# Optimization experiments

Hardware: AMD Instinct MI355X
Metric: run time of the kernel (lower is better)

The kernel has to match this reference:

```python
import jax, jax.numpy as jnp
import numpy as np

C = 256
NUM_GROUPS = 32
EPS = 1e-5


def group_norm(x, gamma, beta):
    # x: [B, C, H, W]; normalize within each of NUM_GROUPS channel groups
    B, Cc, H, W = x.shape
    xg = x.reshape(B, NUM_GROUPS, Cc // NUM_GROUPS, H, W)
    mean = xg.mean(axis=(2, 3, 4), keepdims=True)
    var = xg.var(axis=(2, 3, 4), keepdims=True)
    xg = (xg - mean) * jax.lax.rsqrt(var + EPS)
    x = xg.reshape(B, Cc, H, W)
    return x * gamma[None, :, None, None] + beta[None, :, None, None]


def conv1x1(x, w, b):
    # w: [C_out, C_in], b: [C_out]; equivalent to nn.Conv2d(k=1)
    return jnp.einsum('oc,bchw->bohw', w, x) + b[None, :, None, None]


def setup_inputs() -> dict:
    key = jax.random.key(0)
    ks = jax.random.split(key, 12)
    B, H, W = 8, 64, 64
    x = jax.random.normal(ks[0], (B, C, H, W), dtype=jnp.float32)
    temb = jax.random.normal(ks[1], (B, 512), dtype=jnp.float32)
    s = 1.0 / np.sqrt(C)  # kaiming-uniform-ish scale for 1x1 conv
    def wmat(k):
        return jax.random.uniform(k, (C, C), dtype=jnp.float32, minval=-s, maxval=s)
    def bvec(k):
        return jax.random.uniform(k, (C,), dtype=jnp.float32, minval=-s, maxval=s)
    return {
        'x': x, 'temb': temb,
        'gn_w': jnp.ones((C,), jnp.float32), 'gn_b': jnp.zeros((C,), jnp.float32),
        'wq': wmat(ks[2]), 'bq': bvec(ks[3]),
        'wk': wmat(ks[4]), 'bk': bvec(ks[5]),
        'wv': wmat(ks[6]), 'bv': bvec(ks[7]),
        'wp': wmat(ks[8]), 'bp': bvec(ks[9]),
    }


def reference(x, temb, gn_w, gn_b, wq, bq, wk, bk, wv, bv, wp, bp):
    B, Cc, H, W = x.shape
    h = group_norm(x, gn_w, gn_b)
    q = conv1x1(h, wq, bq)
    k = conv1x1(h, wk, bk)
    v = conv1x1(h, wv, bv)
    # full self-attention over spatial positions: scores [B, H, W, H, W]
    scale = Cc ** (-0.5)
    w = jnp.einsum('bchw,bcij->bhwij', q, k) * scale
    w = jax.nn.softmax(w.reshape(B, H, W, H * W), axis=-1).reshape(B, H, W, H, W)
    h = jnp.einsum('bhwij,bcij->bchw', w, v)
    h = conv1x1(h, wp, bp)
    return (x + h, temb)
```

## Files before the change

kernel.cpp:

```cpp
#include <hip/hip_runtime.h>
#include <hip/hip_bf16.h>

#define B_ 8
#define C_ 256
#define S_ 4096
#define G_ 32
#define GC_ 8
#define EPS_ 1e-5f

typedef __attribute__((ext_vector_type(4))) float f32x4;
typedef __attribute__((ext_vector_type(8))) short bf16x8;
typedef __attribute__((ext_vector_type(4))) short bf16x4;
typedef __attribute__((ext_vector_type(4))) unsigned int u32x4;
typedef __attribute__((ext_vector_type(2))) unsigned int u32x2;

#define DI __device__ __forceinline__

DI unsigned short f2bf(float f) {
    union { float f; unsigned u; } v; v.f = f;
    unsigned r = v.u + 0x7fffu + ((v.u >> 16) & 1u);
    return (unsigned short)(r >> 16);
}

DI unsigned cvt_pk_bf16(float lo, float hi) {
    unsigned r;
    asm("v_cvt_pk_bf16_f32 %0, %1, %2" : "=v"(r) : "v"(lo), "v"(hi));
    return r;
}

__global__ __launch_bounds__(256) void k_gn_stats(const float* __restrict__ x,
                                                  float* __restrict__ stats) {
    int bg = blockIdx.x;
    const float4* xp = (const float4*)(x + (size_t)bg * (GC_ * S_));
    float s = 0.f, ss = 0.f;
    for (int i = threadIdx.x; i < GC_ * S_ / 4; i += 256) {
        float4 v = xp[i];
        s  += v.x + v.y + v.z + v.w;
        ss += v.x * v.x + v.y * v.y + v.z * v.z + v.w * v.w;
    }
    #pragma unroll
    for (int off = 32; off; off >>= 1) { s += __shfl_down(s, off); ss += __shfl_down(ss, off); }
    __shared__ float rs[4], rss[4];
    int w = threadIdx.x >> 6;
    if ((threadIdx.x & 63) == 0) { rs[w] = s; rss[w] = ss; }
    __syncthreads();
    if (threadIdx.x == 0) {
        float S1 = rs[0] + rs[1] + rs[2] + rs[3];
        float S2 = rss[0] + rss[1] + rss[2] + rss[3];
        float inv = 1.f / (GC_ * S_);
        float mean = S1 * inv;
        float var = S2 * inv - mean * mean;
        stats[bg * 2] = mean;
        stats[bg * 2 + 1] = rsqrtf(var + EPS_);
    }
}

__global__ __launch_bounds__(256) void k_gn_apply(const float* __restrict__ x,
                                                  const float* __restrict__ stats,
                                                  const float* __restrict__ gw,
                                                  const float* __restrict__ gb,
                                                  unsigned short* __restrict__ h) {
    int b = blockIdx.x >> 6;
    int s0 = (blockIdx.x & 63) * 64;
    __shared__ unsigned short tile[64 * 256];
    const float* xb = x + (size_t)b * C_ * S_;
    for (int id = threadIdx.x; id < 256 * 16; id += 256) {
        int c = id >> 4, s4 = id & 15;
        float4 v = *(const float4*)(xb + (size_t)c * S_ + s0 + s4 * 4);
        float mean = stats[(b * G_ + (c >> 3)) * 2];
        float rstd = stats[(b * G_ + (c >> 3)) * 2 + 1];
        float ga = gw[c], be = gb[c];
        float vv[4] = {v.x, v.y, v.z, v.w};
        #pragma unroll
        for (int i = 0; i < 4; i++) {
            int srow = s4 * 4 + i;
            unsigned byte = srow * 512u + c * 2u;
            byte ^= ((srow & 7u) << 4);
            *(unsigned short*)((char*)tile + byte) = f2bf((vv[i] - mean) * rstd * ga + be);
        }
    }
    __syncthreads();
    unsigned short* hb = h + (size_t)b * S_ * C_;
    for (int id = threadIdx.x; id < 2048; id += 256) {
        int srow = id >> 5, ck = id & 31;
        unsigned byte = srow * 512u + ck * 16u;
        byte ^= ((srow & 7u) << 4);
        u32x4 v = *(u32x4*)((char*)tile + byte);
        *(u32x4*)(hb + (size_t)(s0 + srow) * C_ + ck * 8) = v;
    }
}

template <int MODE>
__global__ __launch_bounds__(256) void k_gemm(const float* __restrict__ W,
                                              const float* __restrict__ bias,
                                              const unsigned short* __restrict__ Bm,
                                              unsigned short* __restrict__ outb,
                                              float* __restrict__ outf,
                                              const float* __restrict__ xres,
                                              float qscale) {
    int n0 = (blockIdx.x & 31) * 128;
    int m0 = ((blockIdx.x >> 5) & 1) * 128;
    int b = blockIdx.x >> 6;
    __shared__ unsigned short Alds[128 * 64];
    __shared__ unsigned short Blds[128 * 64];
    int tid = threadIdx.x;
    int lane = tid & 63, wv = tid >> 6;
    int wm = (wv >> 1) * 64, wn = (wv & 1) * 64;
    int lr = lane & 15, lg = lane >> 4;
    f32x4 acc[4][4] = {};
    const unsigned short* Bb = Bm + (size_t)b * S_ * C_;

    for (int k0 = 0; k0 < 256; k0 += 64) {
        __syncthreads();
        {
            int row = tid >> 1, half = tid & 1;
            const float* src = W + (size_t)(m0 + row) * C_ + k0 + half * 32;
            unsigned short tmp[32];
            #pragma unroll
            for (int i = 0; i < 8; i++) {
                float4 v = *(const float4*)(src + i * 4);
                tmp[i * 4 + 0] = f2bf(v.x); tmp[i * 4 + 1] = f2bf(v.y);
                tmp[i * 4 + 2] = f2bf(v.z); tmp[i * 4 + 3] = f2bf(v.w);
            }
            #pragma unroll
            for (int i = 0; i < 4; i++) {
                unsigned byte = row * 128u + half * 64u + i * 16u;
                byte ^= ((row & 7u) << 4);
                *(u32x4*)((char*)Alds + byte) = *(u32x4*)(tmp + i * 8);
            }
        }
        #pragma unroll
        for (int i = 0; i < 4; i++) {
            int id = tid + i * 256;
            int row = id >> 3, ck = id & 7;
            u32x4 v = *(const u32x4*)(Bb + (size_t)(n0 + row) * C_ + k0 + ck * 8);
            unsigned byte = row * 128u + ck * 16u;
            byte ^= ((row & 7u) << 4);
            *(u32x4*)((char*)Blds + byte) = v;
        }
        __syncthreads();
        #pragma unroll
        for (int ks = 0; ks < 2; ks++) {
            bf16x8 af[4], bf[4];
            #pragma unroll
            for (int mf = 0; mf < 4; mf++) {
                int m = wm + mf * 16 + lr;
                unsigned byte = m * 128u + ks * 64u + lg * 16u;
                byte ^= ((m & 7u) << 4);
                af[mf] = *(bf16x8*)((char*)Alds + byte);
            }
            #pragma unroll
            for (int nf = 0; nf < 4; nf++) {
                int n = wn + nf * 16 + lr;
                unsigned byte = n * 128u + ks * 64u + lg * 16u;
                byte ^= ((n & 7u) << 4);
                bf[nf] = *(bf16x8*)((char*)Blds + byte);
            }
            #pragma unroll
            for (int mf = 0; mf < 4; mf++)
                #pragma unroll
                for (int nf = 0; nf < 4; nf++)
                    acc[mf][nf] = __builtin_amdgcn_mfma_f32_16x16x32_bf16(af[mf], bf[nf], acc[mf][nf], 0, 0, 0);
        }
    }

    if (MODE == 0 || MODE == 1) {
        unsigned short* ob = outb + (size_t)b * S_ * C_;
        #pragma unroll
        for (int mf = 0; mf < 4; mf++)
            #pragma unroll
            for (int nf = 0; nf < 4; nf++) {
                int cbase = m0 + wm + mf * 16 + lg * 4;
                int srow = n0 + wn + nf * 16 + lr;
                bf16x4 pk;
                #pragma unroll
                for (int r = 0; r < 4; r++) {
                    float v = acc[mf][nf][r] + bias[cbase + r];
                    if (MODE == 0) v *= qscale;
                    pk[r] = (short)f2bf(v);
                }
                *(bf16x4*)(ob + (size_t)srow * C_ + cbase) = pk;
            }
    } else if (MODE == 2) {
        unsigned short* ob = outb + (size_t)b * C_ * S_;
        #pragma unroll
        for (int mf = 0; mf < 4; mf++)
            #pragma unroll
            for (int nf = 0; nf < 4; nf++)
                #pragma unroll
                for (int r = 0; r < 4; r++) {
                    int c = m0 + wm + mf * 16 + lg * 4 + r;
                    int s = n0 + wn + nf * 16 + lr;
                    ob[(size_t)c * S_ + s] = f2bf(acc[mf][nf][r] + bias[c]);
                }
    } else {
        float* ob = outf + (size_t)b * C_ * S_;
        const float* xb = xres + (size_t)b * C_ * S_;
        #pragma unroll
        for (int mf = 0; mf < 4; mf++)
            #pragma unroll
            for (int nf = 0; nf < 4; nf++)
                #pragma unroll
                for (int r = 0; r < 4; r++) {
                    int c = m0 + wm + mf * 16 + lg * 4 + r;
                    int s = n0 + wn + nf * 16 + lr;
                    ob[(size_t)c * S_ + s] = acc[mf][nf][r] + bias[c] + xb[(size_t)c * S_ + s];
                }
    }
}

__global__ __launch_bounds__(512, 2) void k_attn(const unsigned short* __restrict__ Q,
                                                 const unsigned short* __restrict__ K,
                                                 const unsigned short* __restrict__ V,
                                                 unsigned short* __restrict__ O) {
    int b = blockIdx.x & 7;
    int q0 = (blockIdx.x >> 3) * 128;
    int tid = threadIdx.x, lane = tid & 63, wv = tid >> 6;
    int lr = lane & 15, lg = lane >> 4;
    int qg = wv & 3, kg = wv >> 2;
    int qw = q0 + qg * 32;
    __shared__ unsigned short Klds[64 * 256];
    __shared__ unsigned short Vlds[256 * 64];
    __shared__ unsigned short Plds[4][32 * 64];
    __shared__ float mlp[8 * 2 * 16];
    const unsigned short* Qb = Q + (size_t)b * S_ * C_;
    const unsigned short* Kb = K + (size_t)b * S_ * C_;
    const unsigned short* Vb = V + (size_t)b * C_ * S_;

    bf16x8 qf_[8][2];
    #pragma unroll
    for (int ks = 0; ks < 8; ks++)
        #pragma unroll
        for (int qf = 0; qf < 2; qf++)
            qf_[ks][qf] = *(const bf16x8*)(Qb + (size_t)(qw + qf * 16 + lr) * C_ + ks * 32 + lg * 8);

    unsigned kaddr[2][8];
    #pragma unroll
    for (int kf = 0; kf < 2; kf++) {
        int key = kg * 32 + kf * 16 + lr;
        #pragma unroll
        for (int ks = 0; ks < 8; ks++)
            kaddr[kf][ks] = (unsigned)key * 512u + (((unsigned)(4 * ks + lg + 2 * key) & 31u) << 4);
    }

    f32x4 acc[8][2] = {};
    float lrun[2] = {0.f, 0.f};

    int krow[4], kck[4], vc[4], vck[4];
    #pragma unroll
    for (int i = 0; i < 4; i++) {
        int id = tid + i * 512;
        krow[i] = id >> 5; kck[i] = id & 31;
        vc[i] = id >> 3;  vck[i] = id & 7;
    }
    unsigned kwb[4], vwb[4];
    #pragma unroll
    for (int i = 0; i < 4; i++) {
        kwb[i] = krow[i] * 512u + (((unsigned)(kck[i] + 2 * krow[i]) & 31u) << 4);
        vwb[i] = vc[i] * 128u + ((vck[i] * 16u) ^ ((vc[i] & 7u) << 4));
    }

    u32x4 kpre[4], vpre[4];
    #pragma unroll
    for (int i = 0; i < 4; i++) {
        kpre[i] = *(const u32x4*)(Kb + (size_t)krow[i] * C_ + kck[i] * 8);
        vpre[i] = *(const u32x4*)(Vb + (size_t)vc[i] * S_ + vck[i] * 8);
    }
    #pragma unroll
    for (int i = 0; i < 4; i++) {
        *(u32x4*)((char*)Klds + kwb[i]) = kpre[i];
        *(u32x4*)((char*)Vlds + vwb[i]) = vpre[i];
    }
    __syncthreads();

    for (int kt = 0; kt < 64; kt++) {
        bool pf = (kt + 1) < 64;
        if (pf) {
            #pragma unroll
            for (int i = 0; i < 4; i++)
                kpre[i] = *(const u32x4*)(Kb + (size_t)((kt + 1) * 64 + krow[i]) * C_ + kck[i] * 8);
        }

        f32x4 sc[2][2] = {};
        #pragma unroll
        for (int ks = 0; ks < 8; ks++) {
            bf16x8 a[2];
            a[0] = *(const bf16x8*)((char*)Klds + kaddr[0][ks]);
            a[1] = *(const bf16x8*)((char*)Klds + kaddr[1][ks]);
            #pragma unroll
            for (int kf = 0; kf < 2; kf++)
                #pragma unroll
                for (int qf = 0; qf < 2; qf++)
                    sc[kf][qf] = __builtin_amdgcn_mfma_f32_16x16x32_bf16(a[kf], qf_[ks][qf], sc[kf][qf], 0, 0, 0);
        }

        #pragma unroll
        for (int qf = 0; qf < 2; qf++)
            #pragma unroll
            for (int kf = 0; kf < 2; kf++) {
                float p0 = __builtin_amdgcn_exp2f(sc[kf][qf][0] - 16.f);
                float p1 = __builtin_amdgcn_exp2f(sc[kf][qf][1] - 16.f);
                float p2 = __builtin_amdgcn_exp2f(sc[kf][qf][2] - 16.f);
                float p3 = __builtin_amdgcn_exp2f(sc[kf][qf][3] - 16.f);
                lrun[qf] += (p0 + p1) + (p2 + p3);
                u32x2 pk;
                pk[0] = cvt_pk_bf16(p0, p1);
                pk[1] = cvt_pk_bf16(p2, p3);
                int q = qf * 16 + lr;
                unsigned byte = (unsigned)q * 128u + (kg * 32u + kf * 16u + lg * 4u) * 2u;
                byte ^= ((q & 7u) << 4);
                *(u32x2*)((char*)&Plds[qg][0] + byte) = pk;
            }

        if (pf) {
            #pragma unroll
            for (int i = 0; i < 4; i++)
                vpre[i] = *(const u32x4*)(Vb + (size_t)vc[i] * S_ + (kt + 1) * 64 + vck[i] * 8);
        }

        __syncthreads();

        if (pf) {
            #pragma unroll
            for (int i = 0; i < 4; i++)
                *(u32x4*)((char*)Klds + kwb[i]) = kpre[i];
        }

        #pragma unroll
        for (int ks2 = 0; ks2 < 2; ks2++) {
            bf16x8 pb[2];
            #pragma unroll
            for (int qf = 0; qf < 2; qf++) {
                int q = qf * 16 + lr;
                unsigned pbyte = (unsigned)q * 128u + ks2 * 64u + lg * 16u;
                pbyte ^= ((q & 7u) << 4);
                pb[qf] = *(const bf16x8*)((char*)&Plds[qg][0] + pbyte);
            }
            #pragma unroll
            for (int cf = 0; cf < 8; cf++) {
                int c = kg * 128 + cf * 16 + lr;
                unsigned byte = c * 128u + ks2 * 64u + lg * 16u;
                byte ^= ((c & 7u) << 4);
                bf16x8 va = *(const bf16x8*)((char*)Vlds + byte);
                #pragma unroll
                for (int qf = 0; qf < 2; qf++)
                    acc[cf][qf] = __builtin_amdgcn_mfma_f32_16x16x32_bf16(va, pb[qf], acc[cf][qf], 0, 0, 0);
            }
        }

        __syncthreads();

        if (pf) {
            #pragma unroll
            for (int i = 0; i < 4; i++)
                *(u32x4*)((char*)Vlds + vwb[i]) = vpre[i];
        }
    }

    float ls[2];
    #pragma unroll
    for (int qf = 0; qf < 2; qf++) {
        float t = lrun[qf];
        t += __shfl_xor(t, 16);
        t += __shfl_xor(t, 32);
        ls[qf] = t;
    }
    if (lg == 0) {
        #pragma unroll
        for (int qf = 0; qf < 2; qf++) mlp[(wv * 2 + qf) * 16 + lr] = ls[qf];
    }
    __syncthreads();
    unsigned short* Ob = O + (size_t)b * S_ * C_;
    #pragma unroll
    for (int qf = 0; qf < 2; qf++) {
        float inv = 1.f / (ls[qf] + mlp[((wv ^ 4) * 2 + qf) * 16 + lr]);
        int srow = qw + qf * 16 + lr;
        #pragma unroll
        for (int cf = 0; cf < 8; cf++) {
            u32x2 pk;
            pk[0] = cvt_pk_bf16(acc[cf][qf][0] * inv, acc[cf][qf][1] * inv);
            pk[1] = cvt_pk_bf16(acc[cf][qf][2] * inv, acc[cf][qf][3] * inv);
            *(u32x2*)(Ob + (size_t)srow * C_ + kg * 128 + cf * 16 + lg * 4) = pk;
        }
    }
}

__global__ __launch_bounds__(256) void k_copy_temb(const float* __restrict__ t, float* __restrict__ o) {
    int i = blockIdx.x * 256 + threadIdx.x;
    if (i < B_ * 512) o[i] = t[i];
}

extern "C" void kernel_launch(void* const* d_in, const int* in_sizes, int n_in,
                              void* d_out, int out_size, void* d_ws, size_t ws_size,
                              hipStream_t stream) {
    (void)in_sizes; (void)n_in; (void)out_size; (void)ws_size;
    const float* x  = (const float*)d_in[0];
    const float* temb = (const float*)d_in[1];
    const float* gw = (const float*)d_in[2];
    const float* gb = (const float*)d_in[3];
    const float* wq = (const float*)d_in[4];
    const float* bq = (const float*)d_in[5];
    const float* wk = (const float*)d_in[6];
    const float* bk = (const float*)d_in[7];
    const float* wv = (const float*)d_in[8];
    const float* bv = (const float*)d_in[9];
    const float* wp = (const float*)d_in[10];
    const float* bp = (const float*)d_in[11];
    float* out = (float*)d_out;

    char* ws = (char*)d_ws;
    const size_t MB16 = (size_t)B_ * S_ * C_ * 2;
    unsigned short* h_sc = (unsigned short*)ws;
    unsigned short* q_sc = (unsigned short*)(ws + MB16);
    unsigned short* k_sc = (unsigned short*)(ws + 2 * MB16);
    unsigned short* v_cs = (unsigned short*)(ws + 3 * MB16);
    float* stats = (float*)(ws + 4 * MB16);

    const float qscale = 0.0625f * 1.4426950408889634f;

    k_gn_stats<<<B_ * G_, 256, 0, stream>>>(x, stats);
    k_gn_apply<<<B_ * (S_ / 64), 256, 0, stream>>>(x, stats, gw, gb, h_sc);
    k_gemm<0><<<512, 256, 0, stream>>>(wq, bq, h_sc, q_sc, nullptr, nullptr, qscale);
    k_gemm<1><<<512, 256, 0, stream>>>(wk, bk, h_sc, k_sc, nullptr, nullptr, 1.f);
    k_gemm<2><<<512, 256, 0, stream>>>(wv, bv, h_sc, v_cs, nullptr, nullptr, 1.f);
    k_attn<<<B_ * (S_ / 128), 512, 0, stream>>>(q_sc, k_sc, v_cs, h_sc);
    k_gemm<3><<<512, 256, 0, stream>>>(wp, bp, h_sc, nullptr, out, x, 1.f);
    k_copy_temb<<<(B_ * 512 + 255) / 256, 256, 0, stream>>>(temb, out + (size_t)B_ * C_ * S_);
}
```

Before: 226.0 us.

## Pre-convert weights to bf16 once and merge Q/K/V projections into one launch

Adds a small kernel that converts all four fp32 weight matrices to bf16 in workspace once per call, so the GEMM kernels load bf16 weights directly instead of converting fp32 in every tile. The three separate Q/K/V GEMM launches become one 1536-block launch, and block indexing now puts the batch index in the low bits. This cuts per-tile conversion work and launch overhead at the cost of one extra tiny kernel and a workspace region. The attention kernel itself, which dominates runtime, is unchanged.

```diff
diff --git a/kernel.cpp b/kernel.cpp
--- a/kernel.cpp
+++ b/kernel.cpp
@@ -90,17 +90,134 @@
     }
 }
 
-template <int MODE>
-__global__ __launch_bounds__(256) void k_gemm(const float* __restrict__ W,
+__global__ __launch_bounds__(256) void k_wcvt(const float* __restrict__ wq, const float* __restrict__ wk,
+                                              const float* __restrict__ wv, const float* __restrict__ wp,
+                                              unsigned short* __restrict__ wbf) {
+    int t = blockIdx.x * 256 + threadIdx.x;
+    int mat = t >> 13;
+    int idx = (t & 8191) * 8;
+    const float* src = mat == 0 ? wq : mat == 1 ? wk : mat == 2 ? wv : wp;
+    float4 a = *(const float4*)(src + idx);
+    float4 c = *(const float4*)(src + idx + 4);
+    unsigned short tmp[8] = {f2bf(a.x), f2bf(a.y), f2bf(a.z), f2bf(a.w),
+                             f2bf(c.x), f2bf(c.y), f2bf(c.z), f2bf(c.w)};
+    *(u32x4*)(wbf + mat * 65536 + idx) = *(u32x4*)tmp;
+}
+
+__global__ __launch_bounds__(256) void k_qkv(const unsigned short* __restrict__ wbf,
+                                             const float* __restrict__ bq,
+                                             const float* __restrict__ bk,
+                                             const float* __restrict__ bv,
+                                             const unsigned short* __restrict__ h,
+                                             unsigned short* __restrict__ q_sc,
+                                             unsigned short* __restrict__ k_sc,
+                                             unsigned short* __restrict__ v_cs,
+                                             float qscale) {
+    int mode = blockIdx.x >> 9;
+    int inner = blockIdx.x & 511;
+    int b = inner & 7;
+    int rest = inner >> 3;
+    int m0 = (rest & 1) * 128;
+    int n0 = (rest >> 1) * 128;
+    const unsigned short* W = wbf + mode * 65536;
+    const float* bias = mode == 0 ? bq : (mode == 1 ? bk : bv);
+
+    __shared__ unsigned short Alds[128 * 64];
+    __shared__ unsigned short Blds[128 * 64];
+    int tid = threadIdx.x;
+    int lane = tid & 63, wv = tid >> 6;
+    int wm = (wv >> 1) * 64, wn = (wv & 1) * 64;
+    int lr = lane & 15, lg = lane >> 4;
+    f32x4 acc[4][4] = {};
+    const unsigned short* Bb = h + (size_t)b * S_ * C_;
+
+    for (int k0 = 0; k0 < 256; k0 += 64) {
+        __syncthreads();
+        #pragma unroll
+        for (int i = 0; i < 4; i++) {
+            int id = tid + i * 256;
+            int row = id >> 3, ck = id & 7;
+            u32x4 v = *(const u32x4*)(W + (size_t)(m0 + row) * C_ + k0 + ck * 8);
+            unsigned byte = row * 128u + ck * 16u;
+            byte ^= ((row & 7u) << 4);
+            *(u32x4*)((char*)Alds + byte) = v;
+        }
+        #pragma unroll
+        for (int i = 0; i < 4; i++) {
+            int id = tid + i * 256;
+            int row = id >> 3, ck = id & 7;
+            u32x4 v = *(const u32x4*)(Bb + (size_t)(n0 + row) * C_ + k0 + ck * 8);
+            unsigned byte = row * 128u + ck * 16u;
+            byte ^= ((row & 7u) << 4);
+            *(u32x4*)((char*)Blds + byte) = v;
+        }
+        __syncthreads();
+        #pragma unroll
+        for (int ks = 0; ks < 2; ks++) {
+            bf16x8 af[4], bf[4];
+            #pragma unroll
+            for (int mf = 0; mf < 4; mf++) {
+                int m = wm + mf * 16 + lr;
+                unsigned byte = m * 128u + ks * 64u + lg * 16u;
+                byte ^= ((m & 7u) << 4);
+                af[mf] = *(bf16x8*)((char*)Alds + byte);
+            }
+            #pragma unroll
+            for (int nf = 0; nf < 4; nf++) {
+                int n = wn + nf * 16 + lr;
+                unsigned byte = n * 128u + ks * 64u + lg * 16u;
+                byte ^= ((n & 7u) << 4);
+                bf[nf] = *(bf16x8*)((char*)Blds + byte);
+            }
+            #pragma unroll
+            for (int mf = 0; mf < 4; mf++)
+                #pragma unroll
+                for (int nf = 0; nf < 4; nf++)
+                    acc[mf][nf] = __builtin_amdgcn_mfma_f32_16x16x32_bf16(af[mf], bf[nf], acc[mf][nf], 0, 0, 0);
+        }
+    }
+
+    if (mode < 2) {
+        unsigned short* ob = (mode == 0 ? q_sc : k_sc) + (size_t)b * S_ * C_;
+        float sc = mode == 0 ? qscale : 1.f;
+        #pragma unroll
+        for (int mf = 0; mf < 4; mf++)
+            #pragma unroll
+            for (int nf = 0; nf < 4; nf++) {
+                int cbase = m0 + wm + mf * 16 + lg * 4;
+                int srow = n0 + wn + nf * 16 + lr;
+                bf16x4 pk;
+                #pragma unroll
+                for (int r = 0; r < 4; r++)
+                    pk[r] = (short)f2bf((acc[mf][nf][r] + bias[cbase + r]) * sc);
+                *(bf16x4*)(ob + (size_t)srow * C_ + cbase) = pk;
+            }
+    } else {
+        unsigned short* ob = v_cs + (size_t)b * C_ * S_;
+        #pragma unroll
+        for (int mf = 0; mf < 4; mf++)
+            #pragma unroll
+            for (int nf = 0; nf < 4; nf++)
+                #pragma unroll
+                for (int r = 0; r < 4; r++) {
+                    int c = m0 + wm + mf * 16 + lg * 4 + r;
+                    int s = n0 + wn + nf * 16 + lr;
+                    ob[(size_t)c * S_ + s] = f2bf(acc[mf][nf][r] + bias[c]);
+                }
+    }
+}
+
+__global__ __launch_bounds__(256) void k_proj(const unsigned short* __restrict__ wbf,
                                               const float* __restrict__ bias,
                                               const unsigned short* __restrict__ Bm,
-                                              unsigned short* __restrict__ outb,
                                               float* __restrict__ outf,
-                                              const float* __restrict__ xres,
-                                              float qscale) {
-    int n0 = (blockIdx.x & 31) * 128;
-    int m0 = ((blockIdx.x >> 5) & 1) * 128;
-    int b = blockIdx.x >> 6;
+                                              const float* __restrict__ xres) {
+    int b = blockIdx.x & 7;
+    int rest = blockIdx.x >> 3;
+    int m0 = (rest & 1) * 128;
+    int n0 = (rest >> 1) * 128;
+    const unsigned short* W = wbf + 3 * 65536;
+
     __shared__ unsigned short Alds[128 * 64];
     __shared__ unsigned short Blds[128 * 64];
     int tid = threadIdx.x;
@@ -112,22 +229,14 @@
 
     for (int k0 = 0; k0 < 256; k0 += 64) {
         __syncthreads();
-        {
-            int row = tid >> 1, half = tid & 1;
-            const float* src = W + (size_t)(m0 + row) * C_ + k0 + half * 32;
-            unsigned short tmp[32];
-            #pragma unroll
-            for (int i = 0; i < 8; i++) {
-                float4 v = *(const float4*)(src + i * 4);
-                tmp[i * 4 + 0] = f2bf(v.x); tmp[i * 4 + 1] = f2bf(v.y);
-                tmp[i * 4 + 2] = f2bf(v.z); tmp[i * 4 + 3] = f2bf(v.w);
-            }
-            #pragma unroll
-            for (int i = 0; i < 4; i++) {
-                unsigned byte = row * 128u + half * 64u + i * 16u;
-                byte ^= ((row & 7u) << 4);
-                *(u32x4*)((char*)Alds + byte) = *(u32x4*)(tmp + i * 8);
-            }
+        #pragma unroll
+        for (int i = 0; i < 4; i++) {
+            int id = tid + i * 256;
+            int row = id >> 3, ck = id & 7;
+            u32x4 v = *(const u32x4*)(W + (size_t)(m0 + row) * C_ + k0 + ck * 8);
+            unsigned byte = row * 128u + ck * 16u;
+            byte ^= ((row & 7u) << 4);
+            *(u32x4*)((char*)Alds + byte) = v;
         }
         #pragma unroll
         for (int i = 0; i < 4; i++) {
@@ -164,49 +273,18 @@
         }
     }
 
-    if (MODE == 0 || MODE == 1) {
-        unsigned short* ob = outb + (size_t)b * S_ * C_;
-        #pragma unroll
-        for (int mf = 0; mf < 4; mf++)
-            #pragma unroll
-            for (int nf = 0; nf < 4; nf++) {
-                int cbase = m0 + wm + mf * 16 + lg * 4;
-                int srow = n0 + wn + nf * 16 + lr;
-                bf16x4 pk;
-                #pragma unroll
-                for (int r = 0; r < 4; r++) {
-                    float v = acc[mf][nf][r] + bias[cbase + r];
-                    if (MODE == 0) v *= qscale;
-                    pk[r] = (short)f2bf(v);
-                }
-                *(bf16x4*)(ob + (size_t)srow * C_ + cbase) = pk;
-            }
-    } else if (MODE == 2) {
-        unsigned short* ob = outb + (size_t)b * C_ * S_;
-        #pragma unroll
-        for (int mf = 0; mf < 4; mf++)
-            #pragma unroll
-            for (int nf = 0; nf < 4; nf++)
-                #pragma unroll
-                for (int r = 0; r < 4; r++) {
-                    int c = m0 + wm + mf * 16 + lg * 4 + r;
-                    int s = n0 + wn + nf * 16 + lr;
-                    ob[(size_t)c * S_ + s] = f2bf(acc[mf][nf][r] + bias[c]);
-                }
-    } else {
-        float* ob = outf + (size_t)b * C_ * S_;
-        const float* xb = xres + (size_t)b * C_ * S_;
-        #pragma unroll
-        for (int mf = 0; mf < 4; mf++)
-            #pragma unroll
-            for (int nf = 0; nf < 4; nf++)
-                #pragma unroll
-                for (int r = 0; r < 4; r++) {
-                    int c = m0 + wm + mf * 16 + lg * 4 + r;
-                    int s = n0 + wn + nf * 16 + lr;
-                    ob[(size_t)c * S_ + s] = acc[mf][nf][r] + bias[c] + xb[(size_t)c * S_ + s];
-                }
-    }
+    const float* xb = xres + (size_t)b * C_ * S_;
+    #pragma unroll
+    for (int mf = 0; mf < 4; mf++)
+        #pragma unroll
+        for (int nf = 0; nf < 4; nf++)
+            #pragma unroll
+            for (int r = 0; r < 4; r++) {
+                int c = m0 + wm + mf * 16 + lg * 4 + r;
+                int s = n0 + wn + nf * 16 + lr;
+                outf[(size_t)b * C_ * S_ + (size_t)c * S_ + s] =
+                    acc[mf][nf][r] + bias[c] + xb[(size_t)c * S_ + s];
+            }
 }
 
 __global__ __launch_bounds__(512, 2) void k_attn(const unsigned short* __restrict__ Q,
@@ -415,15 +493,15 @@
     unsigned short* k_sc = (unsigned short*)(ws + 2 * MB16);
     unsigned short* v_cs = (unsigned short*)(ws + 3 * MB16);
     float* stats = (float*)(ws + 4 * MB16);
+    unsigned short* wbf = (unsigned short*)(ws + 4 * MB16 + 4096);
 
     const float qscale = 0.0625f * 1.4426950408889634f;
 
+    k_wcvt<<<128, 256, 0, stream>>>(wq, wk, wv, wp, wbf);
     k_gn_stats<<<B_ * G_, 256, 0, stream>>>(x, stats);
     k_gn_apply<<<B_ * (S_ / 64), 256, 0, stream>>>(x, stats, gw, gb, h_sc);
-    k_gemm<0><<<512, 256, 0, stream>>>(wq, bq, h_sc, q_sc, nullptr, nullptr, qscale);
-    k_gemm<1><<<512, 256, 0, stream>>>(wk, bk, h_sc, k_sc, nullptr, nullptr, 1.f);
-    k_gemm<2><<<512, 256, 0, stream>>>(wv, bv, h_sc, v_cs, nullptr, nullptr, 1.f);
+    k_qkv<<<1536, 256, 0, stream>>>(wbf, bq, bk, bv, h_sc, q_sc, k_sc, v_cs, qscale);
     k_attn<<<B_ * (S_ / 128), 512, 0, stream>>>(q_sc, k_sc, v_cs, h_sc);
-    k_gemm<3><<<512, 256, 0, stream>>>(wp, bp, h_sc, nullptr, out, x, 1.f);
+    k_proj<<<512, 256, 0, stream>>>(wbf, bp, h_sc, out, x);
     k_copy_temb<<<(B_ * 512 + 255) / 256, 256, 0, stream>>>(temb, out + (size_t)B_ * C_ * S_);
 }
```

Result: faster. 213.7 us (-5.4%).
